# Kernel optimization log

Hardware: AMD Instinct MI355X
Metric: run time of the kernel (lower is better)

## Reference

```python
import jax, jax.numpy as jnp
import numpy as np

S, B, D, H, K, M, MEM = 1024, 2, 1024, 16, 64, 4096, 1
T = (MEM + 1) * S  # key length = (mem_len+1)*seq_len


def setup_inputs() -> dict:
    key = jax.random.key(0)
    ks = jax.random.split(key, 16)

    def w(k, shape):  # N(0, 0.02) init as in the torch module
        return jax.random.normal(k, shape, dtype=jnp.float32) * 0.02

    x = jax.random.normal(ks[0], (S, B, D), dtype=jnp.float32)
    p = jax.random.normal(ks[1], (T, B, D), dtype=jnp.float32)
    memory = jax.random.normal(ks[2], (MEM * S, B, D), dtype=jnp.float32)
    u_bias = w(ks[3], (H, K))
    v_bias = w(ks[4], (H, K))
    # Transformer-XL causal mask: query s may attend to keys t <= mem_len*S + s
    t_idx = jnp.arange(T)[None, :]
    s_idx = jnp.arange(S)[:, None]
    mask = jnp.where(t_idx <= MEM * S + s_idx, 0.0, -1e9).astype(jnp.float32)[None]  # [1,S,T]
    return {
        "x": x, "p": p, "mask": mask, "memory": memory,
        "u_bias": u_bias, "v_bias": v_bias,
        "wq_w": w(ks[5], (H * K, D)), "wke_w": w(ks[6], (H * K, D)),
        "wkr_w": w(ks[7], (H * K, D)), "wv_w": w(ks[8], (H * K, D)),
        "wc_w": w(ks[9], (D, H * K)),
        "w1_w": w(ks[10], (M, D)), "w1_b": jnp.zeros((M,), jnp.float32),
        "w2_w": w(ks[11], (D, M)), "w2_b": jnp.zeros((D,), jnp.float32),
        "ln1_g": jnp.ones((D,), jnp.float32), "ln1_b": jnp.zeros((D,), jnp.float32),
        "ln2_g": jnp.ones((D,), jnp.float32), "ln2_b": jnp.zeros((D,), jnp.float32),
    }


def _layernorm(x, g, b, eps=1e-5):
    mu = jnp.mean(x, axis=-1, keepdims=True)
    var = jnp.mean(jnp.square(x - mu), axis=-1, keepdims=True)
    return (x - mu) / jnp.sqrt(var + eps) * g + b


def reference(x, p, mask, memory, u_bias, v_bias,
              wq_w, wke_w, wkr_w, wv_w, wc_w,
              w1_w, w1_b, w2_w, w2_b, ln1_g, ln1_b, ln2_g, ln2_b):
    s_len, b_sz, d = x.shape
    q = (x @ wq_w.T).reshape(s_len, b_sz, H, K)            # [S,B,H,K]
    x_mem = jnp.concatenate([memory, x], axis=0)           # [T,B,D]
    k_e = (x_mem @ wke_w.T).reshape(T, b_sz, H, K)         # content keys
    k_r = (p @ wkr_w.T).reshape(T, b_sz, H, K)             # relative-position keys
    v = (x_mem @ wv_w.T).reshape(T, b_sz, H, K)
    # AC: content score, BD: relative-position score (Transformer-XL)
    ac = jnp.einsum("sbhk,tbhk->bhst", q + u_bias, k_e)
    bd = jnp.einsum("sbhk,tbhk->bhst", q + v_bias, k_r)
    alpha = (ac + bd) / np.sqrt(K).astype(np.float32) + mask[:, None]  # [B,H,S,T]
    alpha = jax.nn.softmax(alpha, axis=-1)
    av = jnp.einsum("bhst,tbhk->sbhk", alpha, v).reshape(s_len, b_sz, H * K)
    u = av @ wc_w.T
    u = _layernorm(u + x, ln1_g, ln1_b)
    z = jax.nn.relu(u @ w1_w.T + w1_b) @ w2_w.T + w2_b
    z = _layernorm(z + u, ln2_g, ln2_b)
    return z
```

## Files before the change

### kernel.cpp

```cpp
#include <hip/hip_runtime.h>
#include <math.h>

#define S_LEN 1024
#define BATCH 2
#define DM 1024
#define NH 16
#define HD 64
#define FFN_DIM 4096
#define RQ 2048
#define RT 4096
#define T_LEN 2048
#define KROW 72
#define NPART 3
#define OPSTR 2097152L

typedef __attribute__((ext_vector_type(8))) short short8;
typedef __attribute__((ext_vector_type(4))) float f32x4;

__device__ __forceinline__ unsigned short f2bf(float f) {
    unsigned u = __builtin_bit_cast(unsigned, f);
    u += 0x7fffu + ((u >> 16) & 1u);
    return (unsigned short)(u >> 16);
}
__device__ __forceinline__ float bf2f(unsigned short s) { return __builtin_bit_cast(float, ((unsigned)s) << 16); }

#define GLD_LDS16(gptr, lptr)                                                                  \
    __builtin_amdgcn_global_load_lds((const __attribute__((address_space(1))) unsigned int*)(gptr), \
                                     (__attribute__((address_space(3))) unsigned int*)(lptr), 16, 0, 0)

__device__ __forceinline__ ushort4 cvt4(float4 v) {
    ushort4 o;
    o.x = f2bf(v.x); o.y = f2bf(v.y); o.z = f2bf(v.z); o.w = f2bf(v.w);
    return o;
}

__global__ void cast_all_kernel(const float* __restrict__ wq, const float* __restrict__ wke,
                                const float* __restrict__ wv, const float* __restrict__ wkr,
                                const float* __restrict__ wc, const float* __restrict__ w1,
                                const float* __restrict__ w2, const float* __restrict__ x,
                                const float* __restrict__ p, const float* __restrict__ mem,
                                unsigned short* __restrict__ wdst, unsigned short* __restrict__ xbf,
                                unsigned short* __restrict__ pbf, unsigned short* __restrict__ xm) {
    const long Q = 256 * 1024;
    const long W = 13 * Q;
    long i = (long)blockIdx.x * blockDim.x + threadIdx.x;
    if (i < W) {
        const float* src; long off;
        if      (i < 1 * Q) { src = wq;  off = 0; }
        else if (i < 2 * Q) { src = wke; off = 1 * Q; }
        else if (i < 3 * Q) { src = wv;  off = 2 * Q; }
        else if (i < 4 * Q) { src = wkr; off = 3 * Q; }
        else if (i < 5 * Q) { src = wc;  off = 4 * Q; }
        else if (i < 9 * Q) { src = w1;  off = 5 * Q; }
        else                { src = w2;  off = 9 * Q; }
        ((ushort4*)wdst)[i] = cvt4(((const float4*)src)[i - off]);
    } else if (i < W + 2 * Q) {
        long j = i - W;
        ((ushort4*)xbf)[j] = cvt4(((const float4*)x)[j]);
    } else if (i < W + 6 * Q) {
        long j = i - W - 2 * Q;
        ((ushort4*)pbf)[j] = cvt4(((const float4*)p)[j]);
    } else {
        long j = i - W - 6 * Q;
        float4 v = (j < 2 * Q) ? ((const float4*)mem)[j] : ((const float4*)x)[j - 2 * Q];
        ((ushort4*)xm)[j] = cvt4(v);
    }
}

#define BM 128
#define BN 128
#define GBK 64
#define PBK 32

__launch_bounds__(256)
__global__ void proj_fused(const unsigned short* __restrict__ xbf, const unsigned short* __restrict__ xmbf,
                           const unsigned short* __restrict__ pbf, const unsigned short* __restrict__ wqb,
                           const unsigned short* __restrict__ wkevb, const unsigned short* __restrict__ wkrb,
                           unsigned short* __restrict__ qo, unsigned short* __restrict__ keo,
                           unsigned short* __restrict__ vTo, unsigned short* __restrict__ kro) {
    __shared__ __align__(16) short As[BM * PBK];
    __shared__ __align__(16) short Bs[BN * PBK];
    const int id0 = blockIdx.x;
    const int id = (id0 & 7) * 112 + (id0 >> 3);
    const unsigned short *A, *B;
    unsigned short *Yb, *Yv = nullptr;
    int bx, by;
    if (id < 128)      { A = xbf;  B = wqb;   Yb = qo;  bx = id & 7;   by = id >> 3; }
    else if (id < 640) { int t = id - 128; A = xmbf; B = wkevb; Yb = keo; Yv = vTo;
                         bx = t & 15; by = t >> 4; }
    else               { int t = id - 640; A = pbf;  B = wkrb;  Yb = kro;
                         bx = t & 7;  by = t >> 3; }
    const int tid = threadIdx.x;
    const int w = tid >> 6, lane = tid & 63;
    const int row0 = by * BM, col0 = bx * BN;
    const int wr = (w >> 1) * 64, wcn = (w & 1) * 64;
    f32x4 acc[4][4] = {};
    const int lrow = lane & 15, quad = lane >> 4;
    for (int k0 = 0; k0 < DM; k0 += PBK) {
        __syncthreads();
#pragma unroll
        for (int i = 0; i < 2; ++i) {
            int c = w * 128 + i * 64 + lane;
            int row = c >> 2, kg = c & 3;
            int kl = (kg - (row >> 1)) & 3;
            GLD_LDS16(A + (long)(row0 + row) * DM + k0 + kl * 8, As + (w * 128 + i * 64) * 8);
            GLD_LDS16(B + (long)(col0 + row) * DM + k0 + kl * 8, Bs + (w * 128 + i * 64) * 8);
        }
        __syncthreads();
        short8 a[4], b[4];
#pragma unroll
        for (int mi = 0; mi < 4; ++mi) {
            int r = wr + mi * 16 + lrow;
            int ph = (quad + (r >> 1)) & 3;
            a[mi] = *(const short8*)&As[r * PBK + ph * 8];
        }
#pragma unroll
        for (int ni = 0; ni < 4; ++ni) {
            int r = wcn + ni * 16 + lrow;
            int ph = (quad + (r >> 1)) & 3;
            b[ni] = *(const short8*)&Bs[r * PBK + ph * 8];
        }
#pragma unroll
        for (int mi = 0; mi < 4; ++mi)
#pragma unroll
            for (int ni = 0; ni < 4; ++ni)
                acc[mi][ni] = __builtin_amdgcn_mfma_f32_16x16x32_bf16(a[mi], b[ni], acc[mi][ni], 0, 0, 0);
    }
    const int mb = row0 + wr + quad * 4;
    const int nb = col0 + wcn + lrow;
    const bool isv = (Yv != nullptr) && (col0 >= 1024);
#pragma unroll
    for (int mi = 0; mi < 4; ++mi)
#pragma unroll
        for (int ni = 0; ni < 4; ++ni) {
            const int r = mb + mi * 16, cc = nb + ni * 16;
#pragma unroll
            for (int reg = 0; reg < 4; ++reg) {
                float val = acc[mi][ni][reg];
                const int rf = r + reg;
                if (isv) {
                    int c2 = cc - 1024;
                    int t = rf >> 1, b2 = rf & 1;
                    int h2 = c2 >> 6, d2 = c2 & 63;
                    Yv[((long)(b2 * NH + h2) * HD + d2) * T_LEN + t] = f2bf(val);
                } else {
                    Yb[(long)rf * DM + cc] = f2bf(val);
                }
            }
        }
}

__launch_bounds__(256)
__global__ void gemm_mfma(const unsigned short* __restrict__ A, const unsigned short* __restrict__ B,
                          const float* __restrict__ bias, float* __restrict__ Yf,
                          unsigned short* __restrict__ Yb, int Kd, int N, int relu,
                          int klen, long pstride) {
    __shared__ __align__(16) short As[BM * GBK];
    __shared__ __align__(16) short Bs[BN * GBK];
    const int nbx = N >> 7;
    const int cpx = gridDim.x >> 3;
    const int bid = ((blockIdx.x & 7) * cpx) + (blockIdx.x >> 3);
    const int per_z = nbx << 4;
    const int z = bid / per_z;
    const int r2 = bid - z * per_z;
    const int by = r2 / nbx, bx = r2 - by * nbx;
    const int tid = threadIdx.x;
    const int w = tid >> 6, lane = tid & 63;
    const int row0 = by * BM, col0 = bx * BN;
    const int kbeg = z * klen;
    const int wr = (w >> 1) * 64, wcn = (w & 1) * 64;
    f32x4 acc[4][4] = {};
    const int lrow = lane & 15, quad = lane >> 4;
    for (int k0 = kbeg; k0 < kbeg + klen; k0 += GBK) {
        __syncthreads();
#pragma unroll
        for (int i = 0; i < 4; ++i) {
            int c = i * 256 + tid;
            int row = c >> 3, ph = c & 7;
            int kl = (ph - row) & 7;
            GLD_LDS16(A + (long)(row0 + row) * Kd + k0 + kl * 8, As + (i * 256 + w * 64) * 8);
            GLD_LDS16(B + (long)(col0 + row) * Kd + k0 + kl * 8, Bs + (i * 256 + w * 64) * 8);
        }
        __syncthreads();
#pragma unroll
        for (int hh = 0; hh < 2; ++hh) {
            short8 a[4], b[4];
#pragma unroll
            for (int mi = 0; mi < 4; ++mi) {
                int r = wr + mi * 16 + lrow;
                int ph = (hh * 4 + quad + r) & 7;
                a[mi] = *(const short8*)&As[r * GBK + ph * 8];
            }
#pragma unroll
            for (int ni = 0; ni < 4; ++ni) {
                int r = wcn + ni * 16 + lrow;
                int ph = (hh * 4 + quad + r) & 7;
                b[ni] = *(const short8*)&Bs[r * GBK + ph * 8];
            }
#pragma unroll
            for (int mi = 0; mi < 4; ++mi)
#pragma unroll
                for (int ni = 0; ni < 4; ++ni)
                    acc[mi][ni] = __builtin_amdgcn_mfma_f32_16x16x32_bf16(a[mi], b[ni], acc[mi][ni], 0, 0, 0);
        }
    }
    const int mb = row0 + wr + quad * 4;
    const int nb = col0 + wcn + lrow;
    float* of = Yf ? Yf + (long)z * pstride : nullptr;
    float bb[4];
#pragma unroll
    for (int ni = 0; ni < 4; ++ni) bb[ni] = bias ? bias[nb + ni * 16] : 0.f;
#pragma unroll
    for (int mi = 0; mi < 4; ++mi)
#pragma unroll
        for (int ni = 0; ni < 4; ++ni) {
            const int r = mb + mi * 16, cc = nb + ni * 16;
#pragma unroll
            for (int reg = 0; reg < 4; ++reg) {
                float val = acc[mi][ni][reg] + bb[ni];
                if (relu) val = fmaxf(val, 0.f);
                if (Yb) Yb[(long)(r + reg) * N + cc] = f2bf(val);
                else    of[(long)(r + reg) * N + cc] = val;
            }
        }
}

__launch_bounds__(256)
__global__ void prep_kernel(const unsigned short* __restrict__ kr,
                            const float* __restrict__ ub, const float* __restrict__ vb,
                            unsigned short* __restrict__ ke_io, float* __restrict__ biasg) {
    const int r = blockIdx.x;
    const int tid = threadIdx.x;
    const int h = tid >> 4, seg = tid & 15;
    ushort4 keu = ((const ushort4*)(ke_io + (long)r * DM))[tid];
    ushort4 kru = ((const ushort4*)(kr + (long)r * DM))[tid];
    float ke0 = bf2f(keu.x), ke1 = bf2f(keu.y), ke2 = bf2f(keu.z), ke3 = bf2f(keu.w);
    float kr0 = bf2f(kru.x), kr1 = bf2f(kru.y), kr2 = bf2f(kru.z), kr3 = bf2f(kru.w);
    float4 u4 = ((const float4*)ub)[tid];
    float4 v4 = ((const float4*)vb)[tid];
    ushort4 s;
    s.x = f2bf((ke0 + kr0) * 0.125f); s.y = f2bf((ke1 + kr1) * 0.125f);
    s.z = f2bf((ke2 + kr2) * 0.125f); s.w = f2bf((ke3 + kr3) * 0.125f);
    ((ushort4*)(ke_io + (long)r * DM))[tid] = s;
    float part = u4.x * ke0 + u4.y * ke1 + u4.z * ke2 + u4.w * ke3
               + v4.x * kr0 + v4.y * kr1 + v4.z * kr2 + v4.w * kr3;
    part += __shfl_xor(part, 1);
    part += __shfl_xor(part, 2);
    part += __shfl_xor(part, 4);
    part += __shfl_xor(part, 8);
    if (seg == 0) {
        const int t = r >> 1, b = r & 1;
        biasg[(b * NH + h) * T_LEN + t] = part * 0.125f;
    }
}

__launch_bounds__(256)
__global__ void attn_mfma(const unsigned short* __restrict__ qg,
                          const unsigned short* __restrict__ ksum,
                          const unsigned short* __restrict__ vT,
                          const float* __restrict__ biasg,
                          float* __restrict__ Op01, float* __restrict__ Op2,
                          float2* __restrict__ mlout) {
    __shared__ __align__(16) unsigned short Ks[64 * KROW];
    __shared__ __align__(16) unsigned short Vs[64 * KROW];
    __shared__ __align__(16) unsigned short Ps[4][16 * KROW];
    const int bid0 = blockIdx.x;
    const int bid = (bid0 & 7) * 192 + (bid0 >> 3);
    const int part = bid >> 9, rid = bid & 511;
    const int stile = rid & 15, h = (rid >> 4) & 15, b = rid >> 8;
    const int tid = threadIdx.x, w = tid >> 6, lane = tid & 63;
    const int L = lane & 15, quad = lane >> 4;
    const int qbase = stile * 64 + w * 16;
    short8 qf0, qf1;
    {
        const unsigned short* qp = qg + ((long)(qbase + L) * 2 + b) * DM + h * HD + quad * 8;
        qf0 = *(const short8*)(qp);
        qf1 = *(const short8*)(qp + 32);
    }
    f32x4 O[4] = {};
    float mrow[4] = {-1e30f, -1e30f, -1e30f, -1e30f};
    float lrow[4] = {0.f, 0.f, 0.f, 0.f};
    const int nch = 17 + stile;
    const float* bias_p = biasg + (long)(b * NH + h) * T_LEN;
    const unsigned short* ks_base = ksum + (long)b * DM + h * HD;
    const unsigned short* vt_base = vT + (long)(b * NH + h) * HD * T_LEN;
    const int c0 = tid, c1 = 256 + tid;
    const int row_a = c0 >> 3, seg_a = c0 & 7;
    const int row_b = c1 >> 3, seg_b = c1 & 7;
    uint4 pk0, pk1, pv0, pv1;
    float pb[4];
    {
        const int tf = part * 64;
        pk0 = *(const uint4*)(ks_base + (long)(tf + row_a) * 2 * DM + seg_a * 8);
        pk1 = *(const uint4*)(ks_base + (long)(tf + row_b) * 2 * DM + seg_b * 8);
        pv0 = *(const uint4*)(vt_base + (long)row_a * T_LEN + tf + seg_a * 8);
        pv1 = *(const uint4*)(vt_base + (long)row_b * T_LEN + tf + seg_b * 8);
#pragma unroll
        for (int kt = 0; kt < 4; ++kt) pb[kt] = bias_p[tf + kt * 16 + L];
    }
    for (int ch = part; ch < nch; ch += NPART) {
        const int t0 = ch * 64;
        __syncthreads();
        *(uint4*)&Ks[row_a * KROW + seg_a * 8] = pk0;
        *(uint4*)&Ks[row_b * KROW + seg_b * 8] = pk1;
        *(uint4*)&Vs[row_a * KROW + seg_a * 8] = pv0;
        *(uint4*)&Vs[row_b * KROW + seg_b * 8] = pv1;
        __syncthreads();
        const bool more = (ch + NPART < nch);
        float pbn[4];
        if (more) {
            const int t1 = t0 + NPART * 64;
            pk0 = *(const uint4*)(ks_base + (long)(t1 + row_a) * 2 * DM + seg_a * 8);
            pk1 = *(const uint4*)(ks_base + (long)(t1 + row_b) * 2 * DM + seg_b * 8);
            pv0 = *(const uint4*)(vt_base + (long)row_a * T_LEN + t1 + seg_a * 8);
            pv1 = *(const uint4*)(vt_base + (long)row_b * T_LEN + t1 + seg_b * 8);
#pragma unroll
            for (int kt = 0; kt < 4; ++kt) pbn[kt] = bias_p[t1 + kt * 16 + L];
        }
        f32x4 S[4] = {};
        __builtin_amdgcn_s_setprio(1);
#pragma unroll
        for (int kt = 0; kt < 4; ++kt) {
            short8 kb0 = *(const short8*)&Ks[(kt * 16 + L) * KROW + quad * 8];
            short8 kb1 = *(const short8*)&Ks[(kt * 16 + L) * KROW + 32 + quad * 8];
            S[kt] = __builtin_amdgcn_mfma_f32_16x16x32_bf16(qf0, kb0, S[kt], 0, 0, 0);
            S[kt] = __builtin_amdgcn_mfma_f32_16x16x32_bf16(qf1, kb1, S[kt], 0, 0, 0);
        }
        __builtin_amdgcn_s_setprio(0);
        float sc[4][4];
        float cm[4] = {-1e30f, -1e30f, -1e30f, -1e30f};
        if (ch != nch - 1) {
#pragma unroll
            for (int kt = 0; kt < 4; ++kt)
#pragma unroll
                for (int reg = 0; reg < 4; ++reg) {
                    float v = S[kt][reg] + pb[kt];
                    sc[kt][reg] = v;
                    cm[reg] = fmaxf(cm[reg], v);
                }
        } else {
#pragma unroll
            for (int kt = 0; kt < 4; ++kt)
#pragma unroll
                for (int reg = 0; reg < 4; ++reg) {
                    float v = S[kt][reg] + pb[kt];
                    if (t0 + kt * 16 + L > 1024 + qbase + quad * 4 + reg) v = -1e30f;
                    sc[kt][reg] = v;
                    cm[reg] = fmaxf(cm[reg], v);
                }
        }
#pragma unroll
        for (int off = 1; off < 16; off <<= 1)
#pragma unroll
            for (int reg = 0; reg < 4; ++reg) cm[reg] = fmaxf(cm[reg], __shfl_xor(cm[reg], off));
        float cf[4];
#pragma unroll
        for (int reg = 0; reg < 4; ++reg) {
            float mn = fmaxf(mrow[reg], cm[reg]);
            cf[reg] = __expf(mrow[reg] - mn);
            mrow[reg] = mn;
            lrow[reg] *= cf[reg];
        }
        float rs[4] = {0.f, 0.f, 0.f, 0.f};
#pragma unroll
        for (int kt = 0; kt < 4; ++kt)
#pragma unroll
            for (int reg = 0; reg < 4; ++reg) {
                float pv = __expf(sc[kt][reg] - mrow[reg]);
                rs[reg] += pv;
                Ps[w][(quad * 4 + reg) * KROW + kt * 16 + L] = f2bf(pv);
            }
#pragma unroll
        for (int off = 1; off < 16; off <<= 1)
#pragma unroll
            for (int reg = 0; reg < 4; ++reg) rs[reg] += __shfl_xor(rs[reg], off);
#pragma unroll
        for (int reg = 0; reg < 4; ++reg) lrow[reg] += rs[reg];
#pragma unroll
        for (int dt = 0; dt < 4; ++dt)
#pragma unroll
            for (int reg = 0; reg < 4; ++reg) O[dt][reg] *= cf[reg];
        short8 pa0 = *(const short8*)&Ps[w][L * KROW + quad * 8];
        short8 pa1 = *(const short8*)&Ps[w][L * KROW + 32 + quad * 8];
        __builtin_amdgcn_s_setprio(1);
#pragma unroll
        for (int dt = 0; dt < 4; ++dt) {
            short8 vb0 = *(const short8*)&Vs[(dt * 16 + L) * KROW + quad * 8];
            short8 vb1 = *(const short8*)&Vs[(dt * 16 + L) * KROW + 32 + quad * 8];
            O[dt] = __builtin_amdgcn_mfma_f32_16x16x32_bf16(pa0, vb0, O[dt], 0, 0, 0);
            O[dt] = __builtin_amdgcn_mfma_f32_16x16x32_bf16(pa1, vb1, O[dt], 0, 0, 0);
        }
        __builtin_amdgcn_s_setprio(0);
        if (more) {
#pragma unroll
            for (int kt = 0; kt < 4; ++kt) pb[kt] = pbn[kt];
        }
    }
    float* ob = (part < 2) ? Op01 + (long)part * OPSTR : Op2;
    const long rbase = ((long)b * NH + h) * S_LEN;
#pragma unroll
    for (int reg = 0; reg < 4; ++reg) {
        const int s = qbase + quad * 4 + reg;
        float* op = ob + (rbase + s) * 64;
#pragma unroll
        for (int dt = 0; dt < 4; ++dt) op[dt * 16 + L] = O[dt][reg];
        if (L == 0) mlout[(long)part * 32768 + rbase + s] = make_float2(mrow[reg], lrow[reg]);
    }
}

__launch_bounds__(256)
__global__ void attn_combine(const float* __restrict__ Op01, const float* __restrict__ Op2,
                             const float2* __restrict__ ml,
                             unsigned short* __restrict__ avout) {
    const int i = blockIdx.x * 256 + threadIdx.x;
    const int d4 = i & 15;
    const int row = i >> 4;
    const int s = row & 1023;
    const int bh = row >> 10;
    const int b = bh >> 4, h = bh & 15;
    float2 m0 = ml[row], m1 = ml[row + 32768], m2 = ml[row + 65536];
    float m = fmaxf(fmaxf(m0.x, m1.x), m2.x);
    float a0 = __expf(m0.x - m), a1 = __expf(m1.x - m), a2 = __expf(m2.x - m);
    float inv = 1.f / (a0 * m0.y + a1 * m1.y + a2 * m2.y);
    a0 *= inv; a1 *= inv; a2 *= inv;
    float4 o0 = ((const float4*)Op01)[(long)row * 16 + d4];
    float4 o1 = ((const float4*)Op01)[((long)row + 32768) * 16 + d4];
    float4 o2 = ((const float4*)Op2)[(long)row * 16 + d4];
    float4 o;
    o.x = a0 * o0.x + a1 * o1.x + a2 * o2.x;
    o.y = a0 * o0.y + a1 * o1.y + a2 * o2.y;
    o.z = a0 * o0.z + a1 * o1.z + a2 * o2.z;
    o.w = a0 * o0.w + a1 * o1.w + a2 * o2.w;
    *(ushort4*)(avout + ((long)s * 2 + b) * DM + h * HD + d4 * 4) = cvt4(o);
}

__launch_bounds__(256)
__global__ void ln_kernel(const float* __restrict__ a0, const float* __restrict__ a1,
                          const float* __restrict__ cb, const float* __restrict__ r,
                          const float* __restrict__ g, const float* __restrict__ be,
                          float* __restrict__ out, unsigned short* __restrict__ outb) {
    const int row = blockIdx.x;
    const int tid = threadIdx.x;
    float4 xa = ((const float4*)(a0 + (long)row * DM))[tid];
    if (a1) {
        float4 x1 = ((const float4*)(a1 + (long)row * DM))[tid];
        xa.x += x1.x; xa.y += x1.y; xa.z += x1.z; xa.w += x1.w;
    }
    if (cb) {
        float4 c4 = ((const float4*)cb)[tid];
        xa.x += c4.x; xa.y += c4.y; xa.z += c4.z; xa.w += c4.w;
    }
    float4 xr = ((const float4*)(r + (long)row * DM))[tid];
    float4 x = make_float4(xa.x + xr.x, xa.y + xr.y, xa.z + xr.z, xa.w + xr.w);
    float s1 = x.x + x.y + x.z + x.w;
    float s2 = x.x * x.x + x.y * x.y + x.z * x.z + x.w * x.w;
#pragma unroll
    for (int off = 32; off > 0; off >>= 1) {
        s1 += __shfl_down(s1, off);
        s2 += __shfl_down(s2, off);
    }
    __shared__ float w1s[4], w2s[4];
    const int wid = tid >> 6;
    if ((tid & 63) == 0) { w1s[wid] = s1; w2s[wid] = s2; }
    __syncthreads();
    float S1 = w1s[0] + w1s[1] + w1s[2] + w1s[3];
    float S2 = w2s[0] + w2s[1] + w2s[2] + w2s[3];
    float mu = S1 * (1.f / 1024.f);
    float var = S2 * (1.f / 1024.f) - mu * mu;
    float rstd = rsqrtf(var + 1e-5f);
    float4 gv = ((const float4*)g)[tid];
    float4 bv = ((const float4*)be)[tid];
    float4 o;
    o.x = (x.x - mu) * rstd * gv.x + bv.x;
    o.y = (x.y - mu) * rstd * gv.y + bv.y;
    o.z = (x.z - mu) * rstd * gv.z + bv.z;
    o.w = (x.w - mu) * rstd * gv.w + bv.w;
    ((float4*)(out + (long)row * DM))[tid] = o;
    if (outb) ((ushort4*)(outb + (long)row * DM))[tid] = cvt4(o);
}

extern "C" void kernel_launch(void* const* d_in, const int* in_sizes, int n_in,
                              void* d_out, int out_size, void* d_ws, size_t ws_size,
                              hipStream_t stream) {
    (void)in_sizes; (void)n_in; (void)out_size; (void)ws_size;
    const float* x    = (const float*)d_in[0];
    const float* p    = (const float*)d_in[1];
    const float* mem  = (const float*)d_in[3];
    const float* ub   = (const float*)d_in[4];
    const float* vb   = (const float*)d_in[5];
    const float* wq   = (const float*)d_in[6];
    const float* wke  = (const float*)d_in[7];
    const float* wkr  = (const float*)d_in[8];
    const float* wv   = (const float*)d_in[9];
    const float* wc   = (const float*)d_in[10];
    const float* w1   = (const float*)d_in[11];
    const float* w1b  = (const float*)d_in[12];
    const float* w2   = (const float*)d_in[13];
    const float* w2b  = (const float*)d_in[14];
    const float* ln1g = (const float*)d_in[15];
    const float* ln1b = (const float*)d_in[16];
    const float* ln2g = (const float*)d_in[17];
    const float* ln2b = (const float*)d_in[18];
    float* out = (float*)d_out;
    float* wsf = (float*)d_ws;
    unsigned short* ws16 = (unsigned short*)d_ws;

    const long HLF = 512 * 1024;
    const long M16 = 1024 * 1024;
    unsigned short* wq_bf   = ws16 + 0 * M16;
    unsigned short* wkev_bf = ws16 + 1 * M16;
    unsigned short* wkr_bf  = ws16 + 3 * M16;
    unsigned short* wc_bf   = ws16 + 4 * M16;
    unsigned short* w1_bf   = ws16 + 5 * M16;
    unsigned short* w2_bf   = ws16 + 9 * M16;
    unsigned short* x_bf   = (unsigned short*)(wsf + 13 * HLF);
    unsigned short* xm_bf  = (unsigned short*)(wsf + 15 * HLF);
    unsigned short* p_bf   = (unsigned short*)(wsf + 19 * HLF);
    unsigned short* q_bf   = (unsigned short*)(wsf + 23 * HLF);
    unsigned short* ke_bf  = (unsigned short*)(wsf + 25 * HLF);
    unsigned short* kr_bf  = (unsigned short*)(wsf + 29 * HLF);
    unsigned short* vT_bf  = (unsigned short*)(wsf + 33 * HLF);
    float* abias           = wsf + 37 * HLF;
    float2* mlpart         = (float2*)(wsf + 13 * HLF);
    float* Op01            = wsf + 15 * HLF;
    float* Op2             = wsf + 29 * HLF;
    unsigned short* avb_bf = (unsigned short*)(wsf + 33 * HLF);
    float* t1p             = wsf + 15 * HLF;
    float* u               = wsf + 25 * HLF;
    unsigned short* u_bf   = (unsigned short*)(wsf + 23 * HLF);
    unsigned short* z1_bf  = (unsigned short*)(wsf + 13 * HLF);
    float* t2p             = wsf + 29 * HLF;
    const long PSTR = (long)2048 * 1024;

    cast_all_kernel<<<23552, 256, 0, stream>>>(wq, wke, wv, wkr, wc, w1, w2, x, p, mem,
                                               ws16, x_bf, p_bf, xm_bf);
    proj_fused<<<896, 256, 0, stream>>>(x_bf, xm_bf, p_bf, wq_bf, wkev_bf, wkr_bf,
                                        q_bf, ke_bf, vT_bf, kr_bf);
    prep_kernel<<<RT, 256, 0, stream>>>(kr_bf, ub, vb, ke_bf, abias);
    attn_mfma<<<512 * NPART, 256, 0, stream>>>(q_bf, ke_bf, vT_bf, abias, Op01, Op2, mlpart);
    attn_combine<<<2048, 256, 0, stream>>>(Op01, Op2, mlpart, avb_bf);
    gemm_mfma<<<256, 256, 0, stream>>>(avb_bf, wc_bf, nullptr, t1p, nullptr,
                                       DM, DM, 0, 512, PSTR);
    ln_kernel<<<RQ, 256, 0, stream>>>(t1p, t1p + PSTR, nullptr, x, ln1g, ln1b, u, u_bf);
    gemm_mfma<<<512, 256, 0, stream>>>(u_bf, w1_bf, w1b, nullptr, z1_bf,
                                       DM, FFN_DIM, 1, DM, 0);
    gemm_mfma<<<256, 256, 0, stream>>>(z1_bf, w2_bf, nullptr, t2p, nullptr,
                                       FFN_DIM, DM, 0, 2048, PSTR);
    ln_kernel<<<RQ, 256, 0, stream>>>(t2p, t2p + PSTR, w2b, u, ln2g, ln2b, out, nullptr);
}
```

Baseline: 377.9 us.

## Raise split-K and attention key partitions to four and reorder block scheduling

```diff
diff --git a/kernel.cpp b/kernel.cpp
--- a/kernel.cpp
+++ b/kernel.cpp
@@ -11,7 +11,7 @@
 #define RT 4096
 #define T_LEN 2048
 #define KROW 72
-#define NPART 3
+#define NPART 4
 #define OPSTR 2097152L
 
 typedef __attribute__((ext_vector_type(8))) short short8;
@@ -80,8 +80,7 @@
                            unsigned short* __restrict__ vTo, unsigned short* __restrict__ kro) {
     __shared__ __align__(16) short As[BM * PBK];
     __shared__ __align__(16) short Bs[BN * PBK];
-    const int id0 = blockIdx.x;
-    const int id = (id0 & 7) * 112 + (id0 >> 3);
+    const int id = blockIdx.x;
     const unsigned short *A, *B;
     unsigned short *Yb, *Yv = nullptr;
     int bx, by;
@@ -152,9 +151,11 @@
 
 __launch_bounds__(256)
 __global__ void gemm_mfma(const unsigned short* __restrict__ A, const unsigned short* __restrict__ B,
-                          const float* __restrict__ bias, float* __restrict__ Yf,
+                          const float* __restrict__ bias,
+                          float* __restrict__ of0, float* __restrict__ of1,
+                          float* __restrict__ of2, float* __restrict__ of3,
                           unsigned short* __restrict__ Yb, int Kd, int N, int relu,
-                          int klen, long pstride) {
+                          int klen) {
     __shared__ __align__(16) short As[BM * GBK];
     __shared__ __align__(16) short Bs[BN * GBK];
     const int nbx = N >> 7;
@@ -206,7 +207,7 @@
     }
     const int mb = row0 + wr + quad * 4;
     const int nb = col0 + wcn + lrow;
-    float* of = Yf ? Yf + (long)z * pstride : nullptr;
+    float* of = (z == 0) ? of0 : (z == 1) ? of1 : (z == 2) ? of2 : of3;
     float bb[4];
 #pragma unroll
     for (int ni = 0; ni < 4; ++ni) bb[ni] = bias ? bias[nb + ni * 16] : 0.f;
@@ -260,14 +261,14 @@
                           const unsigned short* __restrict__ vT,
                           const float* __restrict__ biasg,
                           float* __restrict__ Op01, float* __restrict__ Op2,
-                          float2* __restrict__ mlout) {
+                          float* __restrict__ Op3, float2* __restrict__ mlout) {
     __shared__ __align__(16) unsigned short Ks[64 * KROW];
     __shared__ __align__(16) unsigned short Vs[64 * KROW];
     __shared__ __align__(16) unsigned short Ps[4][16 * KROW];
     const int bid0 = blockIdx.x;
-    const int bid = (bid0 & 7) * 192 + (bid0 >> 3);
+    const int bid = (bid0 & 7) * 256 + (bid0 >> 3);
     const int part = bid >> 9, rid = bid & 511;
-    const int stile = rid & 15, h = (rid >> 4) & 15, b = rid >> 8;
+    const int stile = (rid & 15) ^ 15, h = (rid >> 4) & 15, b = rid >> 8;
     const int tid = threadIdx.x, w = tid >> 6, lane = tid & 63;
     const int L = lane & 15, quad = lane >> 4;
     const int qbase = stile * 64 + w * 16;
@@ -396,7 +397,7 @@
             for (int kt = 0; kt < 4; ++kt) pb[kt] = pbn[kt];
         }
     }
-    float* ob = (part < 2) ? Op01 + (long)part * OPSTR : Op2;
+    float* ob = (part == 0) ? Op01 : (part == 1) ? Op01 + OPSTR : (part == 2) ? Op2 : Op3;
     const long rbase = ((long)b * NH + h) * S_LEN;
 #pragma unroll
     for (int reg = 0; reg < 4; ++reg) {
@@ -410,7 +411,7 @@
 
 __launch_bounds__(256)
 __global__ void attn_combine(const float* __restrict__ Op01, const float* __restrict__ Op2,
-                             const float2* __restrict__ ml,
+                             const float* __restrict__ Op3, const float2* __restrict__ ml,
                              unsigned short* __restrict__ avout) {
     const int i = blockIdx.x * 256 + threadIdx.x;
     const int d4 = i & 15;
@@ -418,34 +419,40 @@
     const int s = row & 1023;
     const int bh = row >> 10;
     const int b = bh >> 4, h = bh & 15;
-    float2 m0 = ml[row], m1 = ml[row + 32768], m2 = ml[row + 65536];
-    float m = fmaxf(fmaxf(m0.x, m1.x), m2.x);
-    float a0 = __expf(m0.x - m), a1 = __expf(m1.x - m), a2 = __expf(m2.x - m);
-    float inv = 1.f / (a0 * m0.y + a1 * m1.y + a2 * m2.y);
-    a0 *= inv; a1 *= inv; a2 *= inv;
+    float2 m0 = ml[row], m1 = ml[row + 32768], m2 = ml[row + 65536], m3 = ml[row + 98304];
+    float m = fmaxf(fmaxf(m0.x, m1.x), fmaxf(m2.x, m3.x));
+    float a0 = __expf(m0.x - m), a1 = __expf(m1.x - m);
+    float a2 = __expf(m2.x - m), a3 = __expf(m3.x - m);
+    float inv = 1.f / (a0 * m0.y + a1 * m1.y + a2 * m2.y + a3 * m3.y);
+    a0 *= inv; a1 *= inv; a2 *= inv; a3 *= inv;
     float4 o0 = ((const float4*)Op01)[(long)row * 16 + d4];
     float4 o1 = ((const float4*)Op01)[((long)row + 32768) * 16 + d4];
     float4 o2 = ((const float4*)Op2)[(long)row * 16 + d4];
+    float4 o3 = ((const float4*)Op3)[(long)row * 16 + d4];
     float4 o;
-    o.x = a0 * o0.x + a1 * o1.x + a2 * o2.x;
-    o.y = a0 * o0.y + a1 * o1.y + a2 * o2.y;
-    o.z = a0 * o0.z + a1 * o1.z + a2 * o2.z;
-    o.w = a0 * o0.w + a1 * o1.w + a2 * o2.w;
+    o.x = a0 * o0.x + a1 * o1.x + a2 * o2.x + a3 * o3.x;
+    o.y = a0 * o0.y + a1 * o1.y + a2 * o2.y + a3 * o3.y;
+    o.z = a0 * o0.z + a1 * o1.z + a2 * o2.z + a3 * o3.z;
+    o.w = a0 * o0.w + a1 * o1.w + a2 * o2.w + a3 * o3.w;
     *(ushort4*)(avout + ((long)s * 2 + b) * DM + h * HD + d4 * 4) = cvt4(o);
 }
 
 __launch_bounds__(256)
 __global__ void ln_kernel(const float* __restrict__ a0, const float* __restrict__ a1,
+                          const float* __restrict__ a2, const float* __restrict__ a3,
                           const float* __restrict__ cb, const float* __restrict__ r,
                           const float* __restrict__ g, const float* __restrict__ be,
                           float* __restrict__ out, unsigned short* __restrict__ outb) {
     const int row = blockIdx.x;
     const int tid = threadIdx.x;
     float4 xa = ((const float4*)(a0 + (long)row * DM))[tid];
-    if (a1) {
-        float4 x1 = ((const float4*)(a1 + (long)row * DM))[tid];
-        xa.x += x1.x; xa.y += x1.y; xa.z += x1.z; xa.w += x1.w;
-    }
+    float4 x1 = ((const float4*)(a1 + (long)row * DM))[tid];
+    float4 x2 = ((const float4*)(a2 + (long)row * DM))[tid];
+    float4 x3 = ((const float4*)(a3 + (long)row * DM))[tid];
+    xa.x += x1.x + x2.x + x3.x;
+    xa.y += x1.y + x2.y + x3.y;
+    xa.z += x1.z + x2.z + x3.z;
+    xa.w += x1.w + x2.w + x3.w;
     if (cb) {
         float4 c4 = ((const float4*)cb)[tid];
         xa.x += c4.x; xa.y += c4.y; xa.z += c4.z; xa.w += c4.w;
@@ -524,27 +531,33 @@
     float2* mlpart         = (float2*)(wsf + 13 * HLF);
     float* Op01            = wsf + 15 * HLF;
     float* Op2             = wsf + 29 * HLF;
+    float* Op3             = wsf + 0 * HLF;
     unsigned short* avb_bf = (unsigned short*)(wsf + 33 * HLF);
-    float* t1p             = wsf + 15 * HLF;
+    float* t1p0            = wsf + 15 * HLF;
+    float* t1p1            = wsf + 19 * HLF;
+    float* t1p2            = wsf + 29 * HLF;
+    float* t1p3            = wsf + 0 * HLF;
     float* u               = wsf + 25 * HLF;
     unsigned short* u_bf   = (unsigned short*)(wsf + 23 * HLF);
     unsigned short* z1_bf  = (unsigned short*)(wsf + 13 * HLF);
-    float* t2p             = wsf + 29 * HLF;
-    const long PSTR = (long)2048 * 1024;
+    float* t2p0            = wsf + 0 * HLF;
+    float* t2p1            = wsf + 4 * HLF;
+    float* t2p2            = wsf + 29 * HLF;
+    float* t2p3            = wsf + 33 * HLF;
 
     cast_all_kernel<<<23552, 256, 0, stream>>>(wq, wke, wv, wkr, wc, w1, w2, x, p, mem,
                                                ws16, x_bf, p_bf, xm_bf);
     proj_fused<<<896, 256, 0, stream>>>(x_bf, xm_bf, p_bf, wq_bf, wkev_bf, wkr_bf,
                                         q_bf, ke_bf, vT_bf, kr_bf);
     prep_kernel<<<RT, 256, 0, stream>>>(kr_bf, ub, vb, ke_bf, abias);
-    attn_mfma<<<512 * NPART, 256, 0, stream>>>(q_bf, ke_bf, vT_bf, abias, Op01, Op2, mlpart);
-    attn_combine<<<2048, 256, 0, stream>>>(Op01, Op2, mlpart, avb_bf);
-    gemm_mfma<<<256, 256, 0, stream>>>(avb_bf, wc_bf, nullptr, t1p, nullptr,
-                                       DM, DM, 0, 512, PSTR);
-    ln_kernel<<<RQ, 256, 0, stream>>>(t1p, t1p + PSTR, nullptr, x, ln1g, ln1b, u, u_bf);
-    gemm_mfma<<<512, 256, 0, stream>>>(u_bf, w1_bf, w1b, nullptr, z1_bf,
-                                       DM, FFN_DIM, 1, DM, 0);
-    gemm_mfma<<<256, 256, 0, stream>>>(z1_bf, w2_bf, nullptr, t2p, nullptr,
-                                       FFN_DIM, DM, 0, 2048, PSTR);
-    ln_kernel<<<RQ, 256, 0, stream>>>(t2p, t2p + PSTR, w2b, u, ln2g, ln2b, out, nullptr);
-}
+    attn_mfma<<<512 * NPART, 256, 0, stream>>>(q_bf, ke_bf, vT_bf, abias, Op01, Op2, Op3, mlpart);
+    attn_combine<<<2048, 256, 0, stream>>>(Op01, Op2, Op3, mlpart, avb_bf);
+    gemm_mfma<<<512, 256, 0, stream>>>(avb_bf, wc_bf, nullptr, t1p0, t1p1, t1p2, t1p3,
+                                       nullptr, DM, DM, 0, 256);
+    ln_kernel<<<RQ, 256, 0, stream>>>(t1p0, t1p1, t1p2, t1p3, nullptr, x, ln1g, ln1b, u, u_bf);
+    gemm_mfma<<<512, 256, 0, stream>>>(u_bf, w1_bf, w1b, nullptr, nullptr, nullptr, nullptr,
+                                       z1_bf, DM, FFN_DIM, 1, DM);
+    gemm_mfma<<<512, 256, 0, stream>>>(z1_bf, w2_bf, nullptr, t2p0, t2p1, t2p2, t2p3,
+                                       nullptr, FFN_DIM, DM, 0, 1024);
+    ln_kernel<<<RQ, 256, 0, stream>>>(t2p0, t2p1, t2p2, t2p3, w2b, u, ln2g, ln2b, out, nullptr);
+}
```

New measurement: 372.1 us. About the same (-1.5%).
